# Kernel optimization log

Measured on AMD Instinct MI355X. Metric: run time of the kernel, lower is better.

Reference implementation:

```python
import jax, jax.numpy as jnp
import numpy as np

E = 768
H = 12
DK = E // H
B = 4
S = 2048
EPS = 1e-5


def setup_inputs() -> dict:
    key = jax.random.key(0)
    ks = jax.random.split(key, 8)
    # xavier_uniform bound for square [E, E] weight
    bound = float(np.sqrt(6.0 / (E + E)))
    def xavier(k):
        return jax.random.uniform(k, (E, E), jnp.float32, -bound, bound)
    return {
        "query": jax.random.normal(ks[0], (B, S, E), jnp.float32),
        "key": jax.random.normal(ks[1], (B, S, E), jnp.float32),
        "value": jax.random.normal(ks[2], (B, S, E), jnp.float32),
        "enc_attn_mask": jax.random.randint(ks[3], (B, S, S), 0, 2).astype(bool),
        "Wq": xavier(ks[4]),
        "Wk": xavier(ks[5]),
        "Wv": xavier(ks[6]),
        "Wo": xavier(ks[7]),
    }


def reference(query, key, value, enc_attn_mask, Wq, Wk, Wv, Wo):
    b, s, _ = query.shape
    # projections (nn.Linear: y = x @ W.T), split heads -> [b, h, s, dk]
    Q = (query @ Wq.T).reshape(b, s, H, DK).transpose(0, 2, 1, 3)
    K = (key @ Wk.T).reshape(b, s, H, DK).transpose(0, 2, 1, 3)
    V = (value @ Wv.T).reshape(b, s, H, DK).transpose(0, 2, 1, 3)
    # scaled dot-product attention with boolean mask (True -> -1e9)
    scores = jnp.einsum("bhqd,bhkd->bhqk", Q, K) / np.sqrt(DK).astype(np.float32)
    scores = jnp.where(enc_attn_mask[:, None, :, :], jnp.float32(-1e9), scores)
    attn = jax.nn.softmax(scores, axis=-1)
    context = jnp.einsum("bhqk,bhkd->bhqd", attn, V)
    context = context.transpose(0, 2, 1, 3).reshape(b, s, E)
    out = context @ Wo.T + query  # residual
    # fresh nn.LayerNorm(E): weight=1, bias=0, eps=1e-5
    mean = jnp.mean(out, axis=-1, keepdims=True)
    var = jnp.var(out, axis=-1, keepdims=True)
    return (out - mean) * jax.lax.rsqrt(var + EPS)
```

## Files before the change

kernel.cpp:

```cpp
#include <hip/hip_runtime.h>
#include <stdint.h>
#include <stddef.h>

#define HN   12
#define SN   2048
#define EN   768
#define DKN  64
#define BATCH 4
#define MROWS 8192

typedef short bf16x8 __attribute__((ext_vector_type(8)));
typedef float f32x4 __attribute__((ext_vector_type(4)));

__device__ __forceinline__ unsigned short f2bf(float f) {
  union { float f; unsigned u; } x; x.f = f;
  unsigned r = x.u + 0x7fffu + ((x.u >> 16) & 1u);
  return (unsigned short)(r >> 16);
}

#if __has_builtin(__builtin_amdgcn_cvt_pk_bf16_f32)
typedef __bf16 bf16v2 __attribute__((ext_vector_type(2)));
__device__ __forceinline__ unsigned pk_bf16(float a, float b) {
  union { bf16v2 v; unsigned u; } c;
  c.v = __builtin_amdgcn_cvt_pk_bf16_f32(a, b);
  return c.u;
}
#else
__device__ __forceinline__ unsigned pk_bf16(float a, float b) {
  return (unsigned)f2bf(a) | ((unsigned)f2bf(b) << 16);
}
#endif

#define GLD_LDS16(gptr, lptr) \
  __builtin_amdgcn_global_load_lds((const __attribute__((address_space(1))) void*)(gptr), \
                                   (__attribute__((address_space(3))) void*)(lptr), 16, 0, 0)

#define NBIG4 1572864
#define NW4   147456
__global__ __launch_bounds__(256) void cvt_all(const float* __restrict__ q,
                                               const float* __restrict__ k,
                                               const float* __restrict__ v,
                                               const float* __restrict__ wq,
                                               const float* __restrict__ wk,
                                               const float* __restrict__ wv,
                                               const float* __restrict__ wo,
                                               unsigned short* __restrict__ dst) {
  const int i = blockIdx.x * 256 + threadIdx.x;
  const float* src;
  int off;
  if (i < 3 * NBIG4) {
    const int r = i / NBIG4;
    src = (r == 0) ? q : (r == 1) ? k : v;
    off = i - r * NBIG4;
  } else {
    const int j = i - 3 * NBIG4;
    const int r = j / NW4;
    src = (r == 0) ? wq : (r == 1) ? wk : (r == 2) ? wv : wo;
    off = j - r * NW4;
  }
  float4 val = ((const float4*)src)[off];
  ushort4 o;
  o.x = f2bf(val.x); o.y = f2bf(val.y); o.z = f2bf(val.z); o.w = f2bf(val.w);
  ((ushort4*)dst)[i] = o;
}

__global__ __launch_bounds__(256) void mask_pack(const int* __restrict__ mask,
                                                 unsigned long long* __restrict__ out) {
  const int row = (blockIdx.x * 256 + threadIdx.x) >> 6;
  const int lane = threadIdx.x & 63;
  const int* mrow = mask + (size_t)row * SN;
  unsigned long long* orow = out + (size_t)row * 32;
  for (int kt = 0; kt < 32; ++kt) {
    int v = mrow[kt * 64 + lane];
    unsigned long long bm = __ballot(v != 0);
    if (lane == 0) orow[kt] = bm;
  }
}

template <int MODE>
__global__ __launch_bounds__(256) void gemm_proj(const unsigned short* __restrict__ X,
                                                 const unsigned short* __restrict__ W,
                                                 void* __restrict__ out,
                                                 const float* __restrict__ residual,
                                                 float scale) {
  __shared__ unsigned short As[128 * 32];
  __shared__ unsigned short Bs[128 * 32];
  const int tid  = threadIdx.x;
  const int wave = tid >> 6;
  const int lane = tid & 63;
  const int quad = lane >> 4;
  const int l16  = lane & 15;
  const int bm = blockIdx.x;
  const int bn = blockIdx.y;
  const int wm = wave & 1;
  const int wn = wave >> 1;

  f32x4 acc[4][4] = {};

  const int srow = lane >> 2;
  const int schk = lane & 3;

  for (int bk = 0; bk < 24; ++bk) {
    __syncthreads();
#pragma unroll
    for (int r = 0; r < 2; ++r) {
      const int rowblk = r * 64 + wave * 16;
      GLD_LDS16(X + (size_t)(bm * 128 + rowblk + srow) * EN + bk * 32 + schk * 8,
                As + rowblk * 32);
      GLD_LDS16(W + (size_t)(bn * 128 + rowblk + srow) * EN + bk * 32 + schk * 8,
                Bs + rowblk * 32);
    }
    __syncthreads();

    bf16x8 af[4], bfr[4];
#pragma unroll
    for (int mt = 0; mt < 4; ++mt)
      af[mt] = *(const bf16x8*)&As[(wm * 64 + mt * 16 + l16) * 32 + quad * 8];
#pragma unroll
    for (int nt = 0; nt < 4; ++nt)
      bfr[nt] = *(const bf16x8*)&Bs[(wn * 64 + nt * 16 + l16) * 32 + quad * 8];
#pragma unroll
    for (int mt = 0; mt < 4; ++mt)
#pragma unroll
      for (int nt = 0; nt < 4; ++nt)
        acc[mt][nt] = __builtin_amdgcn_mfma_f32_16x16x32_bf16(af[mt], bfr[nt], acc[mt][nt], 0, 0, 0);
  }

  const int m0 = bm * 128 + wm * 64;
  const int n0 = bn * 128 + wn * 64;

  if (MODE == 0) {
    unsigned short* O = (unsigned short*)out;
#pragma unroll
    for (int mt = 0; mt < 4; ++mt) {
#pragma unroll
      for (int nt = 0; nt < 4; ++nt) {
        const int n = n0 + nt * 16 + l16;
        const int h = n >> 6, d = n & 63;
#pragma unroll
        for (int r = 0; r < 4; ++r) {
          const int m = m0 + mt * 16 + quad * 4 + r;
          const int b = m >> 11, s = m & 2047;
          O[((size_t)(b * HN + h) * SN + s) * DKN + d] = f2bf(acc[mt][nt][r] * scale);
        }
      }
    }
  } else if (MODE == 1) {
    unsigned short* O = (unsigned short*)out;
#pragma unroll
    for (int mt = 0; mt < 4; ++mt) {
#pragma unroll
      for (int nt = 0; nt < 4; ++nt) {
        const int n = n0 + nt * 16 + l16;
        const int h = n >> 6, d = n & 63;
        const int m = m0 + mt * 16 + quad * 4;
        const int b = m >> 11, s = m & 2047;
        ushort4 pk;
        pk.x = f2bf(acc[mt][nt][0]);
        pk.y = f2bf(acc[mt][nt][1]);
        pk.z = f2bf(acc[mt][nt][2]);
        pk.w = f2bf(acc[mt][nt][3]);
        *(ushort4*)&O[((size_t)(b * HN + h) * DKN + d) * SN + s] = pk;
      }
    }
  } else {
    float* O = (float*)out;
#pragma unroll
    for (int mt = 0; mt < 4; ++mt) {
#pragma unroll
      for (int nt = 0; nt < 4; ++nt) {
        const int n = n0 + nt * 16 + l16;
#pragma unroll
        for (int r = 0; r < 4; ++r) {
          const int m = m0 + mt * 16 + quad * 4 + r;
          const size_t idx = (size_t)m * EN + n;
          O[idx] = acc[mt][nt][r] + residual[idx];
        }
      }
    }
  }
}

__global__ __launch_bounds__(256, 6) void attn_kernel(const unsigned short* __restrict__ Q,
                                                      const unsigned short* __restrict__ K,
                                                      const unsigned short* __restrict__ Vt,
                                                      const unsigned long long* __restrict__ Mbits,
                                                      unsigned short* __restrict__ Ctx) {
  __shared__ unsigned short Ks[64 * 64];
  __shared__ unsigned short Vs[64 * 64];

  const int tid  = threadIdx.x;
  const int wave = tid >> 6, lane = tid & 63;
  const int quad = lane >> 4, l16 = lane & 15;
  const int qt = blockIdx.x, bh = blockIdx.y;
  const int b = bh / HN, h = bh - b * HN;

  const unsigned short* Qp = Q + (size_t)bh * SN * DKN;
  const unsigned short* Kp = K + (size_t)bh * SN * DKN;
  const unsigned short* Vp = Vt + (size_t)bh * DKN * SN;

  const int srow = lane >> 3;
  const int schk = lane & 7;
  const int swsrc = (schk ^ srow) * 8;
  const int c0 = (quad ^ (l16 & 7)) * 8;
  const int quad4 = quad * 4;

  const int y0 = wave * 8 + srow;
  const int y1 = 32 + wave * 8 + srow;
  const int px0 = (y0 & 32) + (((y0 & 15) >> 2) << 3) + ((y0 >> 4) & 1) * 4 + (y0 & 3);
  const int px1 = (y1 & 32) + (((y1 & 15) >> 2) << 3) + ((y1 >> 4) & 1) * 4 + (y1 & 3);

  const int R = qt * 64 + wave * 16 + l16;
  const bf16x8 bq0 = *(const bf16x8*)(Qp + (size_t)R * DKN + quad * 8);
  const bf16x8 bq1 = *(const bf16x8*)(Qp + (size_t)R * DKN + 32 + quad * 8);
  const unsigned long long* Mrow = Mbits + ((size_t)(b * SN + R)) * 32;

  f32x4 o_acc[4] = {};
  float l_loc = 0.0f;
  const int shq = 31 - quad * 8;

  for (int kt = 0; kt < 32; ++kt) {
    __syncthreads();
    {
      const int rb0 = wave * 8, rb1 = 32 + wave * 8;
      GLD_LDS16(Kp + (size_t)(kt * 64 + px0) * DKN + swsrc, Ks + rb0 * 64);
      GLD_LDS16(Kp + (size_t)(kt * 64 + px1) * DKN + swsrc, Ks + rb1 * 64);
      GLD_LDS16(Vp + (size_t)(rb0 + srow) * SN + kt * 64 + swsrc, Vs + rb0 * 64);
      GLD_LDS16(Vp + (size_t)(rb1 + srow) * SN + kt * 64 + swsrc, Vs + rb1 * 64);
    }
    const unsigned long long mw = Mrow[kt];
    __syncthreads();

    f32x4 st[4];
#pragma unroll
    for (int mt = 0; mt < 4; ++mt) {
      const int base = (mt * 16 + l16) * 64;
      const bf16x8 ak0 = *(const bf16x8*)&Ks[base + c0];
      const bf16x8 ak1 = *(const bf16x8*)&Ks[base + (c0 ^ 32)];
      f32x4 c = {};
      c = __builtin_amdgcn_mfma_f32_16x16x32_bf16(ak0, bq0, c, 0, 0, 0);
      c = __builtin_amdgcn_mfma_f32_16x16x32_bf16(ak1, bq1, c, 0, 0, 0);
      st[mt] = c;
    }

    const unsigned lo = (unsigned)mw;
    const unsigned hi = (unsigned)(mw >> 32);
    bf16x8 bp[2];
#pragma unroll
    for (int g = 0; g < 2; ++g) {
      const unsigned w = g ? hi : lo;
      float p[8];
#pragma unroll
      for (int t = 0; t < 2; ++t)
#pragma unroll
        for (int r = 0; r < 4; ++r) {
          const float sv = ((int)(w << (shq - t * 4 - r)) < 0) ? -1e9f : st[g * 2 + t][r];
          p[t * 4 + r] = __builtin_exp2f(sv);
        }
      l_loc += ((p[0] + p[1]) + (p[2] + p[3])) + ((p[4] + p[5]) + (p[6] + p[7]));
      union { unsigned u[4]; bf16x8 v; } pk;
      pk.u[0] = pk_bf16(p[0], p[1]);
      pk.u[1] = pk_bf16(p[2], p[3]);
      pk.u[2] = pk_bf16(p[4], p[5]);
      pk.u[3] = pk_bf16(p[6], p[7]);
      bp[g] = pk.v;
    }

#pragma unroll
    for (int dt = 0; dt < 4; ++dt) {
      const int base = (dt * 16 + l16) * 64;
      const bf16x8 av0 = *(const bf16x8*)&Vs[base + c0];
      const bf16x8 av1 = *(const bf16x8*)&Vs[base + (c0 ^ 32)];
      o_acc[dt] = __builtin_amdgcn_mfma_f32_16x16x32_bf16(av0, bp[0], o_acc[dt], 0, 0, 0);
      o_acc[dt] = __builtin_amdgcn_mfma_f32_16x16x32_bf16(av1, bp[1], o_acc[dt], 0, 0, 0);
    }
  }

  l_loc += __shfl_xor(l_loc, 16, 64);
  l_loc += __shfl_xor(l_loc, 32, 64);
  const float inv = 1.0f / l_loc;

  unsigned short* Crow = Ctx + (size_t)(b * SN + R) * EN + h * 64;
#pragma unroll
  for (int dt = 0; dt < 4; ++dt) {
    ushort4 w;
    w.x = f2bf(o_acc[dt][0] * inv);
    w.y = f2bf(o_acc[dt][1] * inv);
    w.z = f2bf(o_acc[dt][2] * inv);
    w.w = f2bf(o_acc[dt][3] * inv);
    *(ushort4*)&Crow[dt * 16 + quad4] = w;
  }
}

__global__ __launch_bounds__(256) void ln_kernel(const float* __restrict__ X,
                                                 float* __restrict__ Y) {
  const int row = blockIdx.x;
  const int t = threadIdx.x;
  const float* xr = X + (size_t)row * EN;
  float v[3];
  float s = 0.f, ss = 0.f;
#pragma unroll
  for (int i = 0; i < 3; ++i) {
    v[i] = xr[t + i * 256];
    s += v[i];
    ss += v[i] * v[i];
  }
#pragma unroll
  for (int off = 1; off < 64; off <<= 1) {
    s += __shfl_xor(s, off, 64);
    ss += __shfl_xor(ss, off, 64);
  }
  __shared__ float ws_s[4], ws_q[4];
  const int wave = t >> 6, lane = t & 63;
  if (lane == 0) { ws_s[wave] = s; ws_q[wave] = ss; }
  __syncthreads();
  s = ws_s[0] + ws_s[1] + ws_s[2] + ws_s[3];
  ss = ws_q[0] + ws_q[1] + ws_q[2] + ws_q[3];
  const float mean = s * (1.0f / EN);
  const float var = ss * (1.0f / EN) - mean * mean;
  const float rstd = rsqrtf(var + 1e-5f);
  float* yr = Y + (size_t)row * EN;
#pragma unroll
  for (int i = 0; i < 3; ++i) yr[t + i * 256] = (v[i] - mean) * rstd;
}

extern "C" void kernel_launch(void* const* d_in, const int* in_sizes, int n_in,
                              void* d_out, int out_size, void* d_ws, size_t ws_size,
                              hipStream_t stream) {
  (void)in_sizes; (void)n_in; (void)out_size; (void)ws_size;
  const float* query = (const float*)d_in[0];
  const float* key_i = (const float*)d_in[1];
  const float* value = (const float*)d_in[2];
  const int*   mask  = (const int*)d_in[3];
  const float* Wq = (const float*)d_in[4];
  const float* Wk = (const float*)d_in[5];
  const float* Wv = (const float*)d_in[6];
  const float* Wo = (const float*)d_in[7];

  const size_t NBIG = (size_t)MROWS * EN;
  const size_t NW   = (size_t)EN * EN;

  unsigned short* Xq16 = (unsigned short*)d_ws;
  unsigned short* Xk16 = Xq16 + NBIG;
  unsigned short* Xv16 = Xk16 + NBIG;
  unsigned short* Wq16 = Xv16 + NBIG;
  unsigned short* Wk16 = Wq16 + NW;
  unsigned short* Wv16 = Wk16 + NW;
  unsigned short* Wo16 = Wv16 + NW;
  unsigned short* Q16  = Wo16 + NW;
  unsigned short* K16  = Q16 + NBIG;
  unsigned short* Vt16 = K16 + NBIG;
  unsigned short* Ctx16 = Vt16 + NBIG;
  float* OutF = (float*)(Ctx16 + NBIG);
  unsigned long long* Mbits = (unsigned long long*)OutF;

  mask_pack<<<MROWS / 4, 256, 0, stream>>>(mask, Mbits);

  const int ncvt = 3 * NBIG4 + 4 * NW4;
  cvt_all<<<ncvt / 256, 256, 0, stream>>>(query, key_i, value, Wq, Wk, Wv, Wo, Xq16);

  dim3 gg(MROWS / 128, EN / 128);
  gemm_proj<0><<<gg, 256, 0, stream>>>(Xq16, Wq16, Q16, nullptr, 0.125f * 1.44269504088896f);
  gemm_proj<0><<<gg, 256, 0, stream>>>(Xk16, Wk16, K16, nullptr, 1.0f);
  gemm_proj<1><<<gg, 256, 0, stream>>>(Xv16, Wv16, Vt16, nullptr, 1.0f);

  attn_kernel<<<dim3(SN / 64, BATCH * HN), 256, 0, stream>>>(Q16, K16, Vt16, Mbits, Ctx16);

  gemm_proj<2><<<gg, 256, 0, stream>>>(Ctx16, Wo16, OutF, query, 1.0f);

  ln_kernel<<<MROWS, 256, 0, stream>>>(OutF, (float*)d_out);
}
```

Baseline: 383.4 us.

## Split attention key tile across wave pairs and batch QKV projections into one launch

Result: faster. 375.1 us (-2.2%).

```diff
diff --git a/kernel.cpp b/kernel.cpp
--- a/kernel.cpp
+++ b/kernel.cpp
@@ -77,12 +77,10 @@
   }
 }
 
-template <int MODE>
-__global__ __launch_bounds__(256) void gemm_proj(const unsigned short* __restrict__ X,
-                                                 const unsigned short* __restrict__ W,
-                                                 void* __restrict__ out,
-                                                 const float* __restrict__ residual,
-                                                 float scale) {
+__global__ __launch_bounds__(256) void gemm_qkv(const unsigned short* __restrict__ Xb,
+                                                const unsigned short* __restrict__ Wb,
+                                                unsigned short* __restrict__ Ob,
+                                                float qscale) {
   __shared__ unsigned short As[128 * 32];
   __shared__ unsigned short Bs[128 * 32];
   const int tid  = threadIdx.x;
@@ -92,11 +90,15 @@
   const int l16  = lane & 15;
   const int bm = blockIdx.x;
   const int bn = blockIdx.y;
+  const int z  = blockIdx.z;
   const int wm = wave & 1;
   const int wn = wave >> 1;
 
+  const unsigned short* X = Xb + (size_t)z * MROWS * EN;
+  const unsigned short* W = Wb + (size_t)z * EN * EN;
+  unsigned short* O = Ob + (size_t)z * MROWS * EN;
+
   f32x4 acc[4][4] = {};
-
   const int srow = lane >> 2;
   const int schk = lane & 3;
 
@@ -128,9 +130,9 @@
 
   const int m0 = bm * 128 + wm * 64;
   const int n0 = bn * 128 + wn * 64;
-
-  if (MODE == 0) {
-    unsigned short* O = (unsigned short*)out;
+  const float scale = (z == 0) ? qscale : 1.0f;
+
+  if (z < 2) {
 #pragma unroll
     for (int mt = 0; mt < 4; ++mt) {
 #pragma unroll
@@ -145,8 +147,7 @@
         }
       }
     }
-  } else if (MODE == 1) {
-    unsigned short* O = (unsigned short*)out;
+  } else {
 #pragma unroll
     for (int mt = 0; mt < 4; ++mt) {
 #pragma unroll
@@ -163,35 +164,87 @@
         *(ushort4*)&O[((size_t)(b * HN + h) * DKN + d) * SN + s] = pk;
       }
     }
-  } else {
-    float* O = (float*)out;
-#pragma unroll
-    for (int mt = 0; mt < 4; ++mt) {
-#pragma unroll
-      for (int nt = 0; nt < 4; ++nt) {
-        const int n = n0 + nt * 16 + l16;
-#pragma unroll
-        for (int r = 0; r < 4; ++r) {
-          const int m = m0 + mt * 16 + quad * 4 + r;
-          const size_t idx = (size_t)m * EN + n;
-          O[idx] = acc[mt][nt][r] + residual[idx];
-        }
+  }
+}
+
+__global__ __launch_bounds__(256) void gemm_out(const unsigned short* __restrict__ X,
+                                                const unsigned short* __restrict__ W,
+                                                float* __restrict__ O,
+                                                const float* __restrict__ residual) {
+  __shared__ unsigned short As[128 * 32];
+  __shared__ unsigned short Bs[128 * 32];
+  const int tid  = threadIdx.x;
+  const int wave = tid >> 6;
+  const int lane = tid & 63;
+  const int quad = lane >> 4;
+  const int l16  = lane & 15;
+  const int bm = blockIdx.x;
+  const int bn = blockIdx.y;
+  const int wm = wave & 1;
+  const int wn = wave >> 1;
+
+  f32x4 acc[4][4] = {};
+  const int srow = lane >> 2;
+  const int schk = lane & 3;
+
+  for (int bk = 0; bk < 24; ++bk) {
+    __syncthreads();
+#pragma unroll
+    for (int r = 0; r < 2; ++r) {
+      const int rowblk = r * 64 + wave * 16;
+      GLD_LDS16(X + (size_t)(bm * 128 + rowblk + srow) * EN + bk * 32 + schk * 8,
+                As + rowblk * 32);
+      GLD_LDS16(W + (size_t)(bn * 128 + rowblk + srow) * EN + bk * 32 + schk * 8,
+                Bs + rowblk * 32);
+    }
+    __syncthreads();
+
+    bf16x8 af[4], bfr[4];
+#pragma unroll
+    for (int mt = 0; mt < 4; ++mt)
+      af[mt] = *(const bf16x8*)&As[(wm * 64 + mt * 16 + l16) * 32 + quad * 8];
+#pragma unroll
+    for (int nt = 0; nt < 4; ++nt)
+      bfr[nt] = *(const bf16x8*)&Bs[(wn * 64 + nt * 16 + l16) * 32 + quad * 8];
+#pragma unroll
+    for (int mt = 0; mt < 4; ++mt)
+#pragma unroll
+      for (int nt = 0; nt < 4; ++nt)
+        acc[mt][nt] = __builtin_amdgcn_mfma_f32_16x16x32_bf16(af[mt], bfr[nt], acc[mt][nt], 0, 0, 0);
+  }
+
+  const int m0 = bm * 128 + wm * 64;
+  const int n0 = bn * 128 + wn * 64;
+#pragma unroll
+  for (int mt = 0; mt < 4; ++mt) {
+#pragma unroll
+    for (int nt = 0; nt < 4; ++nt) {
+      const int n = n0 + nt * 16 + l16;
+#pragma unroll
+      for (int r = 0; r < 4; ++r) {
+        const int m = m0 + mt * 16 + quad * 4 + r;
+        const size_t idx = (size_t)m * EN + n;
+        O[idx] = acc[mt][nt][r] + residual[idx];
       }
     }
   }
 }
 
-__global__ __launch_bounds__(256, 6) void attn_kernel(const unsigned short* __restrict__ Q,
+__global__ __launch_bounds__(256, 4) void attn_kernel(const unsigned short* __restrict__ Q,
                                                       const unsigned short* __restrict__ K,
                                                       const unsigned short* __restrict__ Vt,
-                                                      const unsigned long long* __restrict__ Mbits,
+                                                      const unsigned* __restrict__ Mbits32,
                                                       unsigned short* __restrict__ Ctx) {
-  __shared__ unsigned short Ks[64 * 64];
-  __shared__ unsigned short Vs[64 * 64];
+  __shared__ __align__(16) unsigned char LDSBUF[64 * 68 * 4];
+  __shared__ float lpart[2][2][16];
+  unsigned short* Ks = (unsigned short*)LDSBUF;
+  unsigned short* Vs = (unsigned short*)(LDSBUF + 8192);
+  float* Cmb = (float*)LDSBUF;
 
   const int tid  = threadIdx.x;
   const int wave = tid >> 6, lane = tid & 63;
   const int quad = lane >> 4, l16 = lane & 15;
+  const int qhalf = wave >> 1, kh = wave & 1;
   const int qt = blockIdx.x, bh = blockIdx.y;
   const int b = bh / HN, h = bh - b * HN;
 
@@ -203,92 +256,114 @@
   const int schk = lane & 7;
   const int swsrc = (schk ^ srow) * 8;
   const int c0 = (quad ^ (l16 & 7)) * 8;
-  const int quad4 = quad * 4;
-
-  const int y0 = wave * 8 + srow;
-  const int y1 = 32 + wave * 8 + srow;
-  const int px0 = (y0 & 32) + (((y0 & 15) >> 2) << 3) + ((y0 >> 4) & 1) * 4 + (y0 & 3);
-  const int px1 = (y1 & 32) + (((y1 & 15) >> 2) << 3) + ((y1 >> 4) & 1) * 4 + (y1 & 3);
-
-  const int R = qt * 64 + wave * 16 + l16;
-  const bf16x8 bq0 = *(const bf16x8*)(Qp + (size_t)R * DKN + quad * 8);
-  const bf16x8 bq1 = *(const bf16x8*)(Qp + (size_t)R * DKN + 32 + quad * 8);
-  const unsigned long long* Mrow = Mbits + ((size_t)(b * SN + R)) * 32;
-
-  f32x4 o_acc[4] = {};
-  float l_loc = 0.0f;
+  const int cv = (((kh << 2) + quad) ^ (l16 & 7)) * 8;
   const int shq = 31 - quad * 8;
 
+  const int pw = wave * 8 + srow;
+  const int yk = (((pw >> 2) & 3) << 3) + ((pw >> 4) << 2) + (pw & 3);
+
+  bf16x8 bq[2][2];
+#pragma unroll
+  for (int qg = 0; qg < 2; ++qg) {
+    const int R = qt * 64 + qhalf * 32 + qg * 16 + l16;
+    bq[qg][0] = *(const bf16x8*)(Qp + (size_t)R * DKN + quad * 8);
+    bq[qg][1] = *(const bf16x8*)(Qp + (size_t)R * DKN + 32 + quad * 8);
+  }
+
+  const unsigned* M0 = Mbits32 + ((size_t)(b * SN + qt * 64 + qhalf * 32 + l16)) * 64 + kh;
+
+  f32x4 o_acc[2][4] = {};
+  f32x4 o_l[2] = {};
+  bf16x8 ones;
+#pragma unroll
+  for (int i = 0; i < 8; ++i) ones[i] = (short)0x3F80;
+
   for (int kt = 0; kt < 32; ++kt) {
     __syncthreads();
-    {
-      const int rb0 = wave * 8, rb1 = 32 + wave * 8;
-      GLD_LDS16(Kp + (size_t)(kt * 64 + px0) * DKN + swsrc, Ks + rb0 * 64);
-      GLD_LDS16(Kp + (size_t)(kt * 64 + px1) * DKN + swsrc, Ks + rb1 * 64);
-      GLD_LDS16(Vp + (size_t)(rb0 + srow) * SN + kt * 64 + swsrc, Vs + rb0 * 64);
-      GLD_LDS16(Vp + (size_t)(rb1 + srow) * SN + kt * 64 + swsrc, Vs + rb1 * 64);
-    }
-    const unsigned long long mw = Mrow[kt];
-    __syncthreads();
-
-    f32x4 st[4];
-#pragma unroll
-    for (int mt = 0; mt < 4; ++mt) {
-      const int base = (mt * 16 + l16) * 64;
-      const bf16x8 ak0 = *(const bf16x8*)&Ks[base + c0];
-      const bf16x8 ak1 = *(const bf16x8*)&Ks[base + (c0 ^ 32)];
-      f32x4 c = {};
-      c = __builtin_amdgcn_mfma_f32_16x16x32_bf16(ak0, bq0, c, 0, 0, 0);
-      c = __builtin_amdgcn_mfma_f32_16x16x32_bf16(ak1, bq1, c, 0, 0, 0);
-      st[mt] = c;
-    }
-
-    const unsigned lo = (unsigned)mw;
-    const unsigned hi = (unsigned)(mw >> 32);
-    bf16x8 bp[2];
-#pragma unroll
-    for (int g = 0; g < 2; ++g) {
-      const unsigned w = g ? hi : lo;
+    GLD_LDS16(Kp + (size_t)(kt * 64 + yk) * DKN + swsrc,              Ks + (wave * 8) * 64);
+    GLD_LDS16(Kp + (size_t)(kt * 64 + 32 + yk) * DKN + swsrc,         Ks + (32 + wave * 8) * 64);
+    GLD_LDS16(Vp + (size_t)(wave * 8 + srow) * SN + kt * 64 + swsrc,      Vs + (wave * 8) * 64);
+    GLD_LDS16(Vp + (size_t)(32 + wave * 8 + srow) * SN + kt * 64 + swsrc, Vs + (32 + wave * 8) * 64);
+    const unsigned m0w = M0[kt * 2];
+    const unsigned m1w = M0[kt * 2 + 16 * 64];
+    __syncthreads();
+
+    bf16x8 ak[2][2];
+#pragma unroll
+    for (int mt = 0; mt < 2; ++mt) {
+      const int base = (kh * 32 + mt * 16 + l16) * 64;
+      ak[mt][0] = *(const bf16x8*)&Ks[base + c0];
+      ak[mt][1] = *(const bf16x8*)&Ks[base + (c0 ^ 32)];
+    }
+
+    f32x4 st[2][2];
+#pragma unroll
+    for (int qg = 0; qg < 2; ++qg)
+#pragma unroll
+      for (int mt = 0; mt < 2; ++mt) {
+        f32x4 c = {};
+        c = __builtin_amdgcn_mfma_f32_16x16x32_bf16(ak[mt][0], bq[qg][0], c, 0, 0, 0);
+        c = __builtin_amdgcn_mfma_f32_16x16x32_bf16(ak[mt][1], bq[qg][1], c, 0, 0, 0);
+        st[qg][mt] = c;
+      }
+
+    bf16x8 av[4];
+#pragma unroll
+    for (int dt = 0; dt < 4; ++dt)
+      av[dt] = *(const bf16x8*)&Vs[(dt * 16 + l16) * 64 + cv];
+
+#pragma unroll
+    for (int qg = 0; qg < 2; ++qg) {
+      const unsigned w = qg ? m1w : m0w;
       float p[8];
 #pragma unroll
-      for (int t = 0; t < 2; ++t)
+      for (int mt = 0; mt < 2; ++mt)
 #pragma unroll
         for (int r = 0; r < 4; ++r) {
-          const float sv = ((int)(w << (shq - t * 4 - r)) < 0) ? -1e9f : st[g * 2 + t][r];
-          p[t * 4 + r] = __builtin_exp2f(sv);
+          const float sv = ((int)(w << (shq - mt * 4 - r)) < 0) ? -1e9f : st[qg][mt][r];
+          p[mt * 4 + r] = __builtin_exp2f(sv);
         }
-      l_loc += ((p[0] + p[1]) + (p[2] + p[3])) + ((p[4] + p[5]) + (p[6] + p[7]));
       union { unsigned u[4]; bf16x8 v; } pk;
       pk.u[0] = pk_bf16(p[0], p[1]);
       pk.u[1] = pk_bf16(p[2], p[3]);
       pk.u[2] = pk_bf16(p[4], p[5]);
       pk.u[3] = pk_bf16(p[6], p[7]);
-      bp[g] = pk.v;
-    }
-
-#pragma unroll
-    for (int dt = 0; dt < 4; ++dt) {
-      const int base = (dt * 16 + l16) * 64;
-      const bf16x8 av0 = *(const bf16x8*)&Vs[base + c0];
-      const bf16x8 av1 = *(const bf16x8*)&Vs[base + (c0 ^ 32)];
-      o_acc[dt] = __builtin_amdgcn_mfma_f32_16x16x32_bf16(av0, bp[0], o_acc[dt], 0, 0, 0);
-      o_acc[dt] = __builtin_amdgcn_mfma_f32_16x16x32_bf16(av1, bp[1], o_acc[dt], 0, 0, 0);
-    }
-  }
-
-  l_loc += __shfl_xor(l_loc, 16, 64);
-  l_loc += __shfl_xor(l_loc, 32, 64);
-  const float inv = 1.0f / l_loc;
-
-  unsigned short* Crow = Ctx + (size_t)(b * SN + R) * EN + h * 64;
-#pragma unroll
-  for (int dt = 0; dt < 4; ++dt) {
-    ushort4 w;
-    w.x = f2bf(o_acc[dt][0] * inv);
-    w.y = f2bf(o_acc[dt][1] * inv);
-    w.z = f2bf(o_acc[dt][2] * inv);
-    w.w = f2bf(o_acc[dt][3] * inv);
-    *(ushort4*)&Crow[dt * 16 + quad4] = w;
+      o_l[qg] = __builtin_amdgcn_mfma_f32_16x16x32_bf16(ones, pk.v, o_l[qg], 0, 0, 0);
+#pragma unroll
+      for (int dt = 0; dt < 4; ++dt)
+        o_acc[qg][dt] = __builtin_amdgcn_mfma_f32_16x16x32_bf16(av[dt], pk.v, o_acc[qg][dt], 0, 0, 0);
+    }
+  }
+
+  __syncthreads();
+  if (kh == 1) {
+#pragma unroll
+    for (int qg = 0; qg < 2; ++qg) {
+#pragma unroll
+      for (int dt = 0; dt < 4; ++dt)
+        *(f32x4*)&Cmb[(qhalf * 32 + qg * 16 + l16) * 68 + dt * 16 + quad * 4] = o_acc[qg][dt];
+      if (quad == 0) lpart[qhalf][qg][l16] = o_l[qg][0];
+    }
+  }
+  __syncthreads();
+  if (kh == 0) {
+#pragma unroll
+    for (int qg = 0; qg < 2; ++qg) {
+      const float l = o_l[qg][0] + lpart[qhalf][qg][l16];
+      const float inv = 1.0f / l;
+      const int R = qt * 64 + qhalf * 32 + qg * 16 + l16;
+      unsigned short* Crow = Ctx + (size_t)(b * SN + R) * EN + h * 64;
+#pragma unroll
+      for (int dt = 0; dt < 4; ++dt) {
+        const f32x4 part = *(const f32x4*)&Cmb[(qhalf * 32 + qg * 16 + l16) * 68 + dt * 16 + quad * 4];
+        ushort4 wst;
+        wst.x = f2bf((o_acc[qg][dt][0] + part[0]) * inv);
+        wst.y = f2bf((o_acc[qg][dt][1] + part[1]) * inv);
+        wst.z = f2bf((o_acc[qg][dt][2] + part[2]) * inv);
+        wst.w = f2bf((o_acc[qg][dt][3] + part[3]) * inv);
+        *(ushort4*)&Crow[dt * 16 + quad * 4] = wst;
+      }
+    }
   }
 }
 
@@ -341,12 +416,8 @@
   const size_t NW   = (size_t)EN * EN;
 
   unsigned short* Xq16 = (unsigned short*)d_ws;
-  unsigned short* Xk16 = Xq16 + NBIG;
-  unsigned short* Xv16 = Xk16 + NBIG;
-  unsigned short* Wq16 = Xv16 + NBIG;
-  unsigned short* Wk16 = Wq16 + NW;
-  unsigned short* Wv16 = Wk16 + NW;
-  unsigned short* Wo16 = Wv16 + NW;
+  unsigned short* Wq16 = Xq16 + 3 * NBIG;
+  unsigned short* Wo16 = Wq16 + 3 * NW;
   unsigned short* Q16  = Wo16 + NW;
   unsigned short* K16  = Q16 + NBIG;
   unsigned short* Vt16 = K16 + NBIG;
@@ -359,14 +430,13 @@
   const int ncvt = 3 * NBIG4 + 4 * NW4;
   cvt_all<<<ncvt / 256, 256, 0, stream>>>(query, key_i, value, Wq, Wk, Wv, Wo, Xq16);
 
-  dim3 gg(MROWS / 128, EN / 128);
-  gemm_proj<0><<<gg, 256, 0, stream>>>(Xq16, Wq16, Q16, nullptr, 0.125f * 1.44269504088896f);
-  gemm_proj<0><<<gg, 256, 0, stream>>>(Xk16, Wk16, K16, nullptr, 1.0f);
-  gemm_proj<1><<<gg, 256, 0, stream>>>(Xv16, Wv16, Vt16, nullptr, 1.0f);
-
-  attn_kernel<<<dim3(SN / 64, BATCH * HN), 256, 0, stream>>>(Q16, K16, Vt16, Mbits, Ctx16);
-
-  gemm_proj<2><<<gg, 256, 0, stream>>>(Ctx16, Wo16, OutF, query, 1.0f);
+  gemm_qkv<<<dim3(MROWS / 128, EN / 128, 3), 256, 0, stream>>>(
+      Xq16, Wq16, Q16, 0.125f * 1.44269504088896f);
+
+  attn_kernel<<<dim3(SN / 64, BATCH * HN), 256, 0, stream>>>(
+      Q16, K16, Vt16, (const unsigned*)Mbits, Ctx16);
+
+  gemm_out<<<dim3(MROWS / 128, EN / 128), 256, 0, stream>>>(Ctx16, Wo16, OutF, query);
 
   ln_kernel<<<MROWS, 256, 0, stream>>>(OutF, (float*)d_out);
 }
```
